# Optimization experiments

Hardware: AMD Instinct MI355X
Metric: run time of the kernel (lower is better)

Reference implementation:

```python
import jax, jax.numpy as jnp
import numpy as np

B, CIN, NF, COUT, H, W = 128, 64, 16, 256, 20, 20


def _warp(features, f):
    # features: (B, Cin, r, c), f: (r, c, 2) flow offsets
    r, c = features.shape[2], features.shape[3]
    grid = jnp.stack(
        jnp.meshgrid(jnp.arange(r, dtype=f.dtype), jnp.arange(c, dtype=f.dtype), indexing='ij'),
        axis=-1,
    )  # (r, c, 2) base index map
    idx = grid + f  # index_map += inverse, inverse == flow[i] after double negation
    base = jnp.floor(idx)
    frac = jax.lax.stop_gradient(idx - base)  # torch detaches s and t
    s, t = frac[..., 0], frac[..., 1]
    b = base.astype(jnp.int32)
    bx, by = b[..., 0], b[..., 1]
    padded = jnp.pad(features, ((0, 0), (0, 0), (1, 1), (1, 1)))  # zero pad by 1

    def gather(ix, iy):
        cx = jnp.clip(ix, 0, r)
        cy = jnp.clip(iy, 0, c)
        return padded[:, :, cx + 1, cy + 1]  # (B, Cin, r, c)

    # NOTE: weight for base_10 is s*(1-t) in the original source (apparent bug,
    # should be (1-s)*t) -- replicated here for faithfulness.
    w00 = (1 - s) * (1 - t)
    w01 = s * (1 - t)
    w10 = s * (1 - t)
    w11 = s * t
    return (gather(bx, by) * w00 + gather(bx + 1, by) * w01
            + gather(bx, by + 1) * w10 + gather(bx + 1, by + 1) * w11)


def setup_inputs() -> dict:
    key = jax.random.key(0)
    k1, k2, k3, k4 = jax.random.split(key, 4)
    x = jax.random.normal(k1, (B, CIN, H, W), dtype=jnp.float32)
    flow = jax.random.normal(k2, (NF, H, W, 2), dtype=jnp.float32)
    combinator = jax.random.normal(k3, (COUT, CIN * NF), dtype=jnp.float32) / np.sqrt(CIN * NF)
    bias = jax.random.normal(k4, (COUT,), dtype=jnp.float32) / np.sqrt(CIN * NF)
    return {"x": x, "flow": flow, "combinator": combinator, "bias": bias}


def reference(x, flow, combinator, bias):
    # per-flow bilinear warp, vectorized over the flow axis
    warped = jax.vmap(lambda f: _warp(x, f))(flow)  # (nf, B, Cin, h, w)
    nf, b, cin, h, w = warped.shape
    # permute(1,3,4,2,0).reshape -> columns ordered channel-major, flow-minor
    feat = warped.transpose(1, 3, 4, 2, 0).reshape(b, h, w, cin * nf)
    out = jnp.einsum('bhwk,ok->bhwo', feat, combinator) + bias
    return out.transpose(0, 3, 1, 2)  # (B, Cout, h, w)
```

## Files before the change

### kernel.cpp

```cpp
#include <hip/hip_runtime.h>
#include <hip/hip_fp16.h>
#include <stdint.h>

#define BATCH 128
#define CIN   64
#define NFLOW 16
#define COUT  256
#define HH    20
#define WW    20
#define NPIX  400
#define KTOT  1024
#define PT    80
#define NPT   5
#define NTH   512
#define NCH   16
#define XBS   66
#define FLS   72

typedef __attribute__((ext_vector_type(8))) short sh8;
typedef __attribute__((ext_vector_type(4))) float f4;

__global__ void prep_w(const float* __restrict__ wg, __half* __restrict__ Wf) {
    int gid = blockIdx.x * 256 + threadIdx.x;
    int j8  = gid & 127;
    int row = gid >> 7;
    int kc16 = j8 >> 2;
    int h    = j8 & 3;
    __half* dst = Wf + ((size_t)(kc16 * 16 + (row >> 4)) * 64 + h * 16 + (row & 15)) * 8;
    #pragma unroll
    for (int j = 0; j < 8; ++j) {
        int kp = j8 * 8 + j;
        int l  = kp & 63;
        int c  = (kp >> 6) * 4 + (l & 3);
        int f  = l >> 2;
        dst[j] = __float2half(wg[(size_t)row * KTOT + c * NFLOW + f]);
    }
}

__global__ __launch_bounds__(NTH, 4) void flow_main(
    const float* __restrict__ xg, const __half* __restrict__ Wf,
    const float* __restrict__ flowg, const float* __restrict__ biasg,
    float* __restrict__ outg)
{
    __shared__ __half xb[NPIX * XBS];
    __shared__ __half fl[2][PT * FLS];

    const int bid0 = blockIdx.x;
    const int bid  = (bid0 & 7) * (BATCH * NPT / 8) + (bid0 >> 3);
    const int b  = bid / NPT;
    const int pt = bid - b * NPT;
    const int p0 = pt * PT;

    const int tid  = threadIdx.x;
    const int wv   = tid >> 6;
    const int lane = tid & 63;
    const int lr   = lane & 15;
    const int lk   = (lane >> 4) * 8;

    {
        const float* xbase = xg + (size_t)b * (CIN * NPIX);
        #pragma unroll
        for (int it = 0; it < 25; ++it) {
            int idx = it * NTH + tid;
            int cp  = idx / NPIX;
            int pix = idx - cp * NPIX;
            float v0 = xbase[(2 * cp)     * NPIX + pix];
            float v1 = xbase[(2 * cp + 1) * NPIX + pix];
            __half2 h = __floats2half2_rn(v0, v1);
            *(uint32_t*)&xb[pix * XBS + 2 * cp] = __builtin_bit_cast(uint32_t, h);
        }
    }

    __half2 w2_[3][4];
    int     pb_[3][4];
    int     fo_[3];
    #pragma unroll
    for (int gi = 0; gi < 3; ++gi) {
        int g = tid + gi * NTH;
        if (g < PT * NFLOW) {
            int p = g >> 4, f = g & 15;
            int gp = p0 + p;
            int i = gp / WW;
            int j = gp - i * WW;
            float fx = flowg[((f * HH + i) * WW + j) * 2 + 0];
            float fy = flowg[((f * HH + i) * WW + j) * 2 + 1];
            float ax = (float)i + fx;
            float ay = (float)j + fy;
            float bx = floorf(ax), by = floorf(ay);
            float s = ax - bx, t = ay - by;
            int ibx = (int)bx, iby = (int)by;
            float w00 = (1.f - s) * (1.f - t);
            float w01 = s * (1.f - t);
            float w10 = s * (1.f - t);
            float w11 = s * t;
            int cx0 = min(max(ibx, 0), HH);
            int cx1 = min(max(ibx + 1, 0), HH);
            int cy0 = min(max(iby, 0), WW);
            int cy1 = min(max(iby + 1, 0), WW);
            int v0 = (cx0 < HH) & (cy0 < WW);
            int v1 = (cx1 < HH) & (cy0 < WW);
            int v2 = (cx0 < HH) & (cy1 < WW);
            int v3 = (cx1 < HH) & (cy1 < WW);
            float fw0 = v0 ? w00 : 0.f;
            float fw1 = v1 ? w01 : 0.f;
            float fw2 = v2 ? w10 : 0.f;
            float fw3 = v3 ? w11 : 0.f;
            w2_[gi][0] = __half2half2(__float2half(fw0));
            w2_[gi][1] = __half2half2(__float2half(fw1));
            w2_[gi][2] = __half2half2(__float2half(fw2));
            w2_[gi][3] = __half2half2(__float2half(fw3));
            pb_[gi][0] = (v0 ? (cx0 * WW + cy0) : 0) * (XBS * 2);
            pb_[gi][1] = (v1 ? (cx1 * WW + cy0) : 0) * (XBS * 2);
            pb_[gi][2] = (v2 ? (cx0 * WW + cy1) : 0) * (XBS * 2);
            pb_[gi][3] = (v3 ? (cx1 * WW + cy1) : 0) * (XBS * 2);
            fo_[gi] = p * FLS + f * 4;
        }
    }

    __syncthreads();

    f4 acc[2][5] = {};

    for (int kc = 0; kc < NCH; ++kc) {
        const sh8* wfp = (const sh8*)Wf + (size_t)(2 * kc * 16 + 2 * wv) * 64 + lane;
        sh8 a00 = wfp[0];
        sh8 a01 = wfp[64];
        sh8 a10 = wfp[1024];
        sh8 a11 = wfp[1088];

        __half* flb = fl[kc & 1];
        const int xoff = kc * 8;
        #pragma unroll
        for (int gi = 0; gi < 3; ++gi) {
            if (tid + gi * NTH < PT * NFLOW) {
                __half2 s01 = __builtin_bit_cast(__half2, 0u);
                __half2 s23 = s01;
                #pragma unroll
                for (int q = 0; q < 4; ++q) {
                    const char* bp = (const char*)xb + pb_[gi][q] + xoff;
                    uint32_t dlo = *(const uint32_t*)bp;
                    uint32_t dhi = *(const uint32_t*)(bp + 4);
                    __half2 wq = w2_[gi][q];
                    s01 = __hfma2(wq, __builtin_bit_cast(__half2, dlo), s01);
                    s23 = __hfma2(wq, __builtin_bit_cast(__half2, dhi), s23);
                }
                uint2 pk;
                pk.x = __builtin_bit_cast(uint32_t, s01);
                pk.y = __builtin_bit_cast(uint32_t, s23);
                *(uint2*)&flb[fo_[gi]] = pk;
            }
        }
        __syncthreads();

        const __half* flr = fl[kc & 1];
        #pragma unroll
        for (int nf = 0; nf < 5; ++nf) {
            sh8 b0 = *(const sh8*)&flr[(nf * 16 + lr) * FLS + lk];
            acc[0][nf] = __builtin_amdgcn_mfma_f32_16x16x32_f16(a00, b0, acc[0][nf], 0, 0, 0);
            acc[1][nf] = __builtin_amdgcn_mfma_f32_16x16x32_f16(a01, b0, acc[1][nf], 0, 0, 0);
            sh8 b1 = *(const sh8*)&flr[(nf * 16 + lr) * FLS + 32 + lk];
            acc[0][nf] = __builtin_amdgcn_mfma_f32_16x16x32_f16(a10, b1, acc[0][nf], 0, 0, 0);
            acc[1][nf] = __builtin_amdgcn_mfma_f32_16x16x32_f16(a11, b1, acc[1][nf], 0, 0, 0);
        }
    }

    float* ob = outg + (size_t)b * (COUT * NPIX) + p0;
    #pragma unroll
    for (int mi = 0; mi < 2; ++mi) {
        #pragma unroll
        for (int r = 0; r < 4; ++r) {
            int m = (wv * 2 + mi) * 16 + (lane >> 4) * 4 + r;
            float bs = biasg[m];
            #pragma unroll
            for (int nf = 0; nf < 5; ++nf)
                ob[(size_t)m * NPIX + nf * 16 + lr] = acc[mi][nf][r] + bs;
        }
    }
}

extern "C" void kernel_launch(void* const* d_in, const int* in_sizes, int n_in,
                              void* d_out, int out_size, void* d_ws, size_t ws_size,
                              hipStream_t stream) {
    const float* x    = (const float*)d_in[0];
    const float* flow = (const float*)d_in[1];
    const float* comb = (const float*)d_in[2];
    const float* bias = (const float*)d_in[3];
    float* out = (float*)d_out;

    __half* Wf = (__half*)d_ws;

    prep_w<<<dim3(128), dim3(256), 0, stream>>>(comb, Wf);
    flow_main<<<dim3(BATCH * NPT), dim3(NTH), 0, stream>>>(x, Wf, flow, bias, out);
}
```

Baseline: 50.10 us.

## Stream x per channel-chunk with double-buffered LDS and reorder K by flow blocks

Instead of staging the whole fp16 image tile (all 64 channels) in LDS up front, the kernel now streams 8 channels per k-chunk into a small double-buffered LDS slab. The next chunk's global loads are issued before the current warp step, hiding their latency. The combinator K ordering is changed to flow-block-major with 8 channels per chunk, so warp tables are rebuilt only twice. Block size is halved to 256 threads, with each wave owning 64 output rows and 4 accumulator sets, and MFMA sections are raised in priority via s_setprio. The aim is to cut LDS footprint and the serial prologue and raise occupancy, at the cost of more global reloads per chunk, higher register pressure and fewer threads doing the gather work.

```diff
diff --git a/kernel.cpp b/kernel.cpp
--- a/kernel.cpp
+++ b/kernel.cpp
@@ -12,9 +12,7 @@
 #define KTOT  1024
 #define PT    80
 #define NPT   5
-#define NTH   512
-#define NCH   16
-#define XBS   66
+#define NTH   256
 #define FLS   72
 
 typedef __attribute__((ext_vector_type(8))) short sh8;
@@ -30,20 +28,21 @@
     #pragma unroll
     for (int j = 0; j < 8; ++j) {
         int kp = j8 * 8 + j;
+        int kc = kp >> 6;
         int l  = kp & 63;
-        int c  = (kp >> 6) * 4 + (l & 3);
-        int f  = l >> 2;
+        int f  = (kc >> 3) * 8 + (l >> 3);
+        int c  = (kc & 7) * 8 + (l & 7);
         dst[j] = __float2half(wg[(size_t)row * KTOT + c * NFLOW + f]);
     }
 }
 
-__global__ __launch_bounds__(NTH, 4) void flow_main(
+__global__ __launch_bounds__(NTH, 3) void flow_main(
     const float* __restrict__ xg, const __half* __restrict__ Wf,
     const float* __restrict__ flowg, const float* __restrict__ biasg,
     float* __restrict__ outg)
 {
-    __shared__ __half xb[NPIX * XBS];
-    __shared__ __half fl[2][PT * FLS];
+    __shared__ __align__(16) __half xc[2][NPIX * 8];
+    __shared__ __align__(16) __half fl[2][PT * FLS];
 
     const int bid0 = blockIdx.x;
     const int bid  = (bid0 & 7) * (BATCH * NPT / 8) + (bid0 >> 3);
@@ -57,119 +56,160 @@
     const int lr   = lane & 15;
     const int lk   = (lane >> 4) * 8;
 
-    {
-        const float* xbase = xg + (size_t)b * (CIN * NPIX);
-        #pragma unroll
-        for (int it = 0; it < 25; ++it) {
-            int idx = it * NTH + tid;
-            int cp  = idx / NPIX;
-            int pix = idx - cp * NPIX;
-            float v0 = xbase[(2 * cp)     * NPIX + pix];
-            float v1 = xbase[(2 * cp + 1) * NPIX + pix];
-            __half2 h = __floats2half2_rn(v0, v1);
-            *(uint32_t*)&xb[pix * XBS + 2 * cp] = __builtin_bit_cast(uint32_t, h);
-        }
-    }
+    const float* xb = xg + (size_t)b * (CIN * NPIX);
 
     __half2 w2_[3][4];
     int     pb_[3][4];
     int     fo_[3];
-    #pragma unroll
-    for (int gi = 0; gi < 3; ++gi) {
-        int g = tid + gi * NTH;
-        if (g < PT * NFLOW) {
-            int p = g >> 4, f = g & 15;
-            int gp = p0 + p;
-            int i = gp / WW;
-            int j = gp - i * WW;
-            float fx = flowg[((f * HH + i) * WW + j) * 2 + 0];
-            float fy = flowg[((f * HH + i) * WW + j) * 2 + 1];
-            float ax = (float)i + fx;
-            float ay = (float)j + fy;
-            float bx = floorf(ax), by = floorf(ay);
-            float s = ax - bx, t = ay - by;
-            int ibx = (int)bx, iby = (int)by;
-            float w00 = (1.f - s) * (1.f - t);
-            float w01 = s * (1.f - t);
-            float w10 = s * (1.f - t);
-            float w11 = s * t;
-            int cx0 = min(max(ibx, 0), HH);
-            int cx1 = min(max(ibx + 1, 0), HH);
-            int cy0 = min(max(iby, 0), WW);
-            int cy1 = min(max(iby + 1, 0), WW);
-            int v0 = (cx0 < HH) & (cy0 < WW);
-            int v1 = (cx1 < HH) & (cy0 < WW);
-            int v2 = (cx0 < HH) & (cy1 < WW);
-            int v3 = (cx1 < HH) & (cy1 < WW);
-            float fw0 = v0 ? w00 : 0.f;
-            float fw1 = v1 ? w01 : 0.f;
-            float fw2 = v2 ? w10 : 0.f;
-            float fw3 = v3 ? w11 : 0.f;
-            w2_[gi][0] = __half2half2(__float2half(fw0));
-            w2_[gi][1] = __half2half2(__float2half(fw1));
-            w2_[gi][2] = __half2half2(__float2half(fw2));
-            w2_[gi][3] = __half2half2(__float2half(fw3));
-            pb_[gi][0] = (v0 ? (cx0 * WW + cy0) : 0) * (XBS * 2);
-            pb_[gi][1] = (v1 ? (cx1 * WW + cy0) : 0) * (XBS * 2);
-            pb_[gi][2] = (v2 ? (cx0 * WW + cy1) : 0) * (XBS * 2);
-            pb_[gi][3] = (v3 ? (cx1 * WW + cy1) : 0) * (XBS * 2);
-            fo_[gi] = p * FLS + f * 4;
-        }
-    }
-
+
+    auto build_tables = [&](int fb) {
+        #pragma unroll
+        for (int gi = 0; gi < 3; ++gi) {
+            int g = tid + gi * NTH;
+            if (g < PT * 8) {
+                int fi = g / PT;
+                int p  = g - fi * PT;
+                int f  = fb * 8 + fi;
+                int gp = p0 + p;
+                int i = gp / WW;
+                int j = gp - i * WW;
+                float fx = flowg[((f * HH + i) * WW + j) * 2 + 0];
+                float fy = flowg[((f * HH + i) * WW + j) * 2 + 1];
+                float ax = (float)i + fx;
+                float ay = (float)j + fy;
+                float bxf = floorf(ax), byf = floorf(ay);
+                float s = ax - bxf, t = ay - byf;
+                int ibx = (int)bxf, iby = (int)byf;
+                float w00 = (1.f - s) * (1.f - t);
+                float w01 = s * (1.f - t);
+                float w10 = s * (1.f - t);
+                float w11 = s * t;
+                int cx0 = min(max(ibx, 0), HH);
+                int cx1 = min(max(ibx + 1, 0), HH);
+                int cy0 = min(max(iby, 0), WW);
+                int cy1 = min(max(iby + 1, 0), WW);
+                int v0 = (cx0 < HH) & (cy0 < WW);
+                int v1 = (cx1 < HH) & (cy0 < WW);
+                int v2 = (cx0 < HH) & (cy1 < WW);
+                int v3 = (cx1 < HH) & (cy1 < WW);
+                w2_[gi][0] = __half2half2(__float2half(v0 ? w00 : 0.f));
+                w2_[gi][1] = __half2half2(__float2half(v1 ? w01 : 0.f));
+                w2_[gi][2] = __half2half2(__float2half(v2 ? w10 : 0.f));
+                w2_[gi][3] = __half2half2(__float2half(v3 ? w11 : 0.f));
+                pb_[gi][0] = (v0 ? (cx0 * WW + cy0) : 0) * 16;
+                pb_[gi][1] = (v1 ? (cx1 * WW + cy0) : 0) * 16;
+                pb_[gi][2] = (v2 ? (cx0 * WW + cy1) : 0) * 16;
+                pb_[gi][3] = (v3 ? (cx1 * WW + cy1) : 0) * 16;
+                fo_[gi] = p * (FLS * 2) + fi * 16;
+            }
+        }
+    };
+
+    {
+        #pragma unroll
+        for (int it = 0; it < 7; ++it) {
+            int idx = it * NTH + tid;
+            if (idx < 1600) {
+                int pix = idx >> 2, q = idx & 3;
+                float v0 = xb[(2 * q)     * NPIX + pix];
+                float v1 = xb[(2 * q + 1) * NPIX + pix];
+                __half2 h = __floats2half2_rn(v0, v1);
+                *(uint32_t*)&xc[0][pix * 8 + 2 * q] = __builtin_bit_cast(uint32_t, h);
+            }
+        }
+    }
+    build_tables(0);
     __syncthreads();
 
-    f4 acc[2][5] = {};
-
-    for (int kc = 0; kc < NCH; ++kc) {
-        const sh8* wfp = (const sh8*)Wf + (size_t)(2 * kc * 16 + 2 * wv) * 64 + lane;
-        sh8 a00 = wfp[0];
-        sh8 a01 = wfp[64];
-        sh8 a10 = wfp[1024];
-        sh8 a11 = wfp[1088];
-
-        __half* flb = fl[kc & 1];
-        const int xoff = kc * 8;
-        #pragma unroll
-        for (int gi = 0; gi < 3; ++gi) {
-            if (tid + gi * NTH < PT * NFLOW) {
-                __half2 s01 = __builtin_bit_cast(__half2, 0u);
-                __half2 s23 = s01;
-                #pragma unroll
-                for (int q = 0; q < 4; ++q) {
-                    const char* bp = (const char*)xb + pb_[gi][q] + xoff;
-                    uint32_t dlo = *(const uint32_t*)bp;
-                    uint32_t dhi = *(const uint32_t*)(bp + 4);
-                    __half2 wq = w2_[gi][q];
-                    s01 = __hfma2(wq, __builtin_bit_cast(__half2, dlo), s01);
-                    s23 = __hfma2(wq, __builtin_bit_cast(__half2, dhi), s23);
+    f4 acc[4][5] = {};
+
+    for (int kc = 0; kc < 16; ++kc) {
+        if (kc == 8) build_tables(1);
+
+        float rv0[7], rv1[7];
+        const int ncb = (kc + 1) & 7;
+        if (kc < 15) {
+            #pragma unroll
+            for (int it = 0; it < 7; ++it) {
+                int idx = it * NTH + tid;
+                if (idx < 1600) {
+                    int pix = idx >> 2, q = idx & 3;
+                    rv0[it] = xb[(ncb * 8 + 2 * q)     * NPIX + pix];
+                    rv1[it] = xb[(ncb * 8 + 2 * q + 1) * NPIX + pix];
                 }
-                uint2 pk;
-                pk.x = __builtin_bit_cast(uint32_t, s01);
-                pk.y = __builtin_bit_cast(uint32_t, s23);
-                *(uint2*)&flb[fo_[gi]] = pk;
-            }
-        }
+            }
+        }
+
+        {
+            const char* xcb = (const char*)xc[kc & 1];
+            char* flb = (char*)fl[kc & 1];
+            #pragma unroll
+            for (int gi = 0; gi < 3; ++gi) {
+                if (tid + gi * NTH < PT * 8) {
+                    __half2 s0 = __builtin_bit_cast(__half2, 0u);
+                    __half2 s1 = s0, s2 = s0, s3 = s0;
+                    #pragma unroll
+                    for (int q = 0; q < 4; ++q) {
+                        const uint4 d = *(const uint4*)(xcb + pb_[gi][q]);
+                        __half2 wq = w2_[gi][q];
+                        s0 = __hfma2(wq, __builtin_bit_cast(__half2, d.x), s0);
+                        s1 = __hfma2(wq, __builtin_bit_cast(__half2, d.y), s1);
+                        s2 = __hfma2(wq, __builtin_bit_cast(__half2, d.z), s2);
+                        s3 = __hfma2(wq, __builtin_bit_cast(__half2, d.w), s3);
+                    }
+                    uint4 pk;
+                    pk.x = __builtin_bit_cast(uint32_t, s0);
+                    pk.y = __builtin_bit_cast(uint32_t, s1);
+                    pk.z = __builtin_bit_cast(uint32_t, s2);
+                    pk.w = __builtin_bit_cast(uint32_t, s3);
+                    *(uint4*)(flb + fo_[gi]) = pk;
+                }
+            }
+        }
+
+        if (kc < 15) {
+            __half* xcn = xc[(kc + 1) & 1];
+            #pragma unroll
+            for (int it = 0; it < 7; ++it) {
+                int idx = it * NTH + tid;
+                if (idx < 1600) {
+                    int pix = idx >> 2, q = idx & 3;
+                    __half2 h = __floats2half2_rn(rv0[it], rv1[it]);
+                    *(uint32_t*)&xcn[pix * 8 + 2 * q] = __builtin_bit_cast(uint32_t, h);
+                }
+            }
+        }
+
+        const sh8* wfp = (const sh8*)Wf + (size_t)(32 * kc + 4 * wv) * 64 + lane;
+        sh8 a0_0 = wfp[0],    a0_1 = wfp[64],   a0_2 = wfp[128],  a0_3 = wfp[192];
+        sh8 a1_0 = wfp[1024], a1_1 = wfp[1088], a1_2 = wfp[1152], a1_3 = wfp[1216];
+
         __syncthreads();
 
         const __half* flr = fl[kc & 1];
+        __builtin_amdgcn_s_setprio(1);
         #pragma unroll
         for (int nf = 0; nf < 5; ++nf) {
             sh8 b0 = *(const sh8*)&flr[(nf * 16 + lr) * FLS + lk];
-            acc[0][nf] = __builtin_amdgcn_mfma_f32_16x16x32_f16(a00, b0, acc[0][nf], 0, 0, 0);
-            acc[1][nf] = __builtin_amdgcn_mfma_f32_16x16x32_f16(a01, b0, acc[1][nf], 0, 0, 0);
+            acc[0][nf] = __builtin_amdgcn_mfma_f32_16x16x32_f16(a0_0, b0, acc[0][nf], 0, 0, 0);
+            acc[1][nf] = __builtin_amdgcn_mfma_f32_16x16x32_f16(a0_1, b0, acc[1][nf], 0, 0, 0);
+            acc[2][nf] = __builtin_amdgcn_mfma_f32_16x16x32_f16(a0_2, b0, acc[2][nf], 0, 0, 0);
+            acc[3][nf] = __builtin_amdgcn_mfma_f32_16x16x32_f16(a0_3, b0, acc[3][nf], 0, 0, 0);
             sh8 b1 = *(const sh8*)&flr[(nf * 16 + lr) * FLS + 32 + lk];
-            acc[0][nf] = __builtin_amdgcn_mfma_f32_16x16x32_f16(a10, b1, acc[0][nf], 0, 0, 0);
-            acc[1][nf] = __builtin_amdgcn_mfma_f32_16x16x32_f16(a11, b1, acc[1][nf], 0, 0, 0);
-        }
+            acc[0][nf] = __builtin_amdgcn_mfma_f32_16x16x32_f16(a1_0, b1, acc[0][nf], 0, 0, 0);
+            acc[1][nf] = __builtin_amdgcn_mfma_f32_16x16x32_f16(a1_1, b1, acc[1][nf], 0, 0, 0);
+            acc[2][nf] = __builtin_amdgcn_mfma_f32_16x16x32_f16(a1_2, b1, acc[2][nf], 0, 0, 0);
+            acc[3][nf] = __builtin_amdgcn_mfma_f32_16x16x32_f16(a1_3, b1, acc[3][nf], 0, 0, 0);
+        }
+        __builtin_amdgcn_s_setprio(0);
     }
 
     float* ob = outg + (size_t)b * (COUT * NPIX) + p0;
     #pragma unroll
-    for (int mi = 0; mi < 2; ++mi) {
+    for (int mi = 0; mi < 4; ++mi) {
         #pragma unroll
         for (int r = 0; r < 4; ++r) {
-            int m = (wv * 2 + mi) * 16 + (lane >> 4) * 4 + r;
+            int m = wv * 64 + mi * 16 + (lane >> 4) * 4 + r;
             float bs = biasg[m];
             #pragma unroll
             for (int nf = 0; nf < 5; ++nf)
```

Result: slower. 68.42 us (+36.6%).
